# Kernel tuning notes

Hardware: AMD Instinct MI355X
Metric: run time of the kernel (lower is better)

The kernel has to match this reference:

```python
import jax, jax.numpy as jnp
import numpy as np

DN = ('NCHW', 'OIHW', 'NCHW')
EPS = 1e-5


def _conv(x, w, b, stride, pad):
    y = jax.lax.conv_general_dilated(x, w, (stride, stride), ((pad, pad), (pad, pad)), dimension_numbers=DN)
    return y + b[None, :, None, None]


def _convT(x, w, b):
    # PyTorch ConvTranspose2d(k=4, s=2, p=1); w: (Cin, Cout, 4, 4)
    k = jnp.flip(w, (2, 3)).transpose(1, 0, 2, 3)  # -> (Cout, Cin, 4, 4)
    y = jax.lax.conv_general_dilated(x, k, (1, 1), ((2, 2), (2, 2)), lhs_dilation=(2, 2), dimension_numbers=DN)
    return y + b[None, :, None, None]


def _bn(x, g, b):
    # training-mode BatchNorm2d: batch stats over (N, H, W)
    m = x.mean((0, 2, 3), keepdims=True)
    v = x.var((0, 2, 3), keepdims=True)
    return (x - m) * jax.lax.rsqrt(v + EPS) * g[None, :, None, None] + b[None, :, None, None]


def _resblock(x, g1, b1, w3, b3, g2, b2, w1, b1c):
    h = jax.nn.relu(_bn(x, g1, b1))
    h = _conv(h, w3, b3, 1, 1)
    h = jax.nn.relu(_bn(h, g2, b2))
    h = _conv(h, w1, b1c, 1, 0)
    return h + x


def setup_inputs() -> dict:
    B, C, H, W, D, K = 16, 3, 128, 128, 256, 512
    key = jax.random.key(0)
    ks = iter(jax.random.split(key, 16))
    s = 0.05
    inp = {
        'x': jax.random.normal(next(ks), (B, C, H, W), jnp.float32),
        'ec1_w': jax.random.normal(next(ks), (D, C, 4, 4), jnp.float32) * s,
        'ec1_b': jnp.zeros((D,), jnp.float32),
        'ebn1_g': jnp.ones((D,), jnp.float32),
        'ebn1_b': jnp.zeros((D,), jnp.float32),
        'ec2_w': jax.random.normal(next(ks), (D, D, 4, 4), jnp.float32) * s,
        'ec2_b': jnp.zeros((D,), jnp.float32),
        # 4 residual blocks stacked: [0,1]=encoder, [2,3]=decoder
        'rb_bn1_g': jnp.ones((4, D), jnp.float32),
        'rb_bn1_b': jnp.zeros((4, D), jnp.float32),
        'rb_c3_w': jax.random.normal(next(ks), (4, D, D, 3, 3), jnp.float32) * s,
        'rb_c3_b': jnp.zeros((4, D), jnp.float32),
        'rb_bn2_g': jnp.ones((4, D), jnp.float32),
        'rb_bn2_b': jnp.zeros((4, D), jnp.float32),
        'rb_c1_w': jax.random.normal(next(ks), (4, D, D, 1, 1), jnp.float32) * s,
        'rb_c1_b': jnp.zeros((4, D), jnp.float32),
        'dbn1_g': jnp.ones((D,), jnp.float32),
        'dbn1_b': jnp.zeros((D,), jnp.float32),
        'dct1_w': jax.random.normal(next(ks), (D, D, 4, 4), jnp.float32) * s,  # (Cin, Cout, kH, kW)
        'dct1_b': jnp.zeros((D,), jnp.float32),
        'dbn2_g': jnp.ones((D,), jnp.float32),
        'dbn2_b': jnp.zeros((D,), jnp.float32),
        'dct2_w': jax.random.normal(next(ks), (D, C, 4, 4), jnp.float32) * s,
        'dct2_b': jnp.zeros((C,), jnp.float32),
        'codebook': jax.random.uniform(next(ks), (K, D), jnp.float32, -1.0 / K, 1.0 / K),
    }
    return inp


def reference(x, ec1_w, ec1_b, ebn1_g, ebn1_b, ec2_w, ec2_b,
              rb_bn1_g, rb_bn1_b, rb_c3_w, rb_c3_b, rb_bn2_g, rb_bn2_b, rb_c1_w, rb_c1_b,
              dbn1_g, dbn1_b, dct1_w, dct1_b, dbn2_g, dbn2_b, dct2_w, dct2_b, codebook):
    def rb(h, i):
        return _resblock(h, rb_bn1_g[i], rb_bn1_b[i], rb_c3_w[i], rb_c3_b[i],
                         rb_bn2_g[i], rb_bn2_b[i], rb_c1_w[i], rb_c1_b[i])

    # Encoder
    h = _conv(x, ec1_w, ec1_b, 2, 1)
    h = jax.nn.relu(_bn(h, ebn1_g, ebn1_b))
    h = _conv(h, ec2_w, ec2_b, 2, 1)
    h = rb(h, 0)
    z_e = rb(h, 1)  # [N, D, H/4, W/4]

    # Vector quantizer: argmin_k sum_d (z - w_k)^2 via norm expansion
    N, D, Hh, Ww = z_e.shape
    ze_f = z_e.transpose(0, 2, 3, 1).reshape(-1, D)  # [M, D]
    d2 = ((ze_f ** 2).sum(1, keepdims=True)
          - 2.0 * ze_f @ codebook.T
          + (codebook ** 2).sum(1)[None, :])  # [M, K]
    q = jnp.argmin(d2, axis=1)
    z_q = codebook[q].reshape(N, Hh, Ww, D).transpose(0, 3, 1, 2)

    # Decoder (takes z_e, per original forward)
    d = rb(z_e, 2)
    d = rb(d, 3)
    d = jax.nn.relu(_bn(d, dbn1_g, dbn1_b))
    d = _convT(d, dct1_w, dct1_b)
    d = jax.nn.relu(_bn(d, dbn2_g, dbn2_b))
    x_rec = _convT(d, dct2_w, dct2_b)

    return (x_rec, z_e, z_q)
```

## Files before the change

kernel.cpp:

```cpp
#include <hip/hip_runtime.h>
#include <stdint.h>

typedef __bf16 bf16_t;
typedef __bf16 bf16x8 __attribute__((ext_vector_type(8)));
typedef float f32x4 __attribute__((ext_vector_type(4)));

#define DEVINL __device__ __forceinline__

DEVINL float bf2f(bf16_t h){ return (float)h; }
DEVINL bf16_t f2bf(float f){ return (bf16_t)f; }

DEVINL void g2l16(const void* g, void* l){
  __builtin_amdgcn_global_load_lds(
      (const __attribute__((address_space(1))) uint32_t*)g,
      (__attribute__((address_space(3))) uint32_t*)l, 16, 0, 0);
}

#define SB_BYTES    9469952
#define SB0_OFF     35684352
#define STATS_OFF   73564160
#define CBN_OFF     73586688
#define WP_OFF      73588736
#define XI_OFF      83320832
#define WS_NEEDED   91709440
#define WP_RB3(i) (1048576 + (i)*655360)
#define WP_RB1(i) (1048576 + (i)*655360 + 589824)
#define WP_CT     3670016
#define WP_CB     4718592
#define WP_EC1    4849664
#define WP_ELEMS  4866048

__global__ __launch_bounds__(256) void k_zero(uint4* __restrict__ p, int n16){
  int i = blockIdx.x*256 + threadIdx.x;
  if (i < n16) p[i] = make_uint4(0,0,0,0);
}

__global__ __launch_bounds__(256) void k_zerohalo(bf16_t* __restrict__ buf, int IW, int total){
  int idx = blockIdx.x*256 + threadIdx.x;
  if (idx >= total) return;
  int g8 = idx & 31, r = idx >> 5;
  int H = 4*IW - 4;
  int nn = r / H, hp = r - nn*H;
  int y, x;
  if (hp < IW){ y = 0; x = hp; }
  else if (hp < 2*IW){ y = IW-1; x = hp - IW; }
  else {
    int h2 = hp - 2*IW;
    int side = h2 / (IW-2);
    int k = h2 - side*(IW-2);
    y = k + 1; x = side ? (IW-1) : 0;
  }
  bf16_t* p = buf + ((size_t)((nn*IW + y)*IW + x))*256 + g8*8;
  bf16x8 zv;
#pragma unroll
  for (int e = 0; e < 8; e++) zv[e] = f2bf(0.f);
  *(bf16x8*)p = zv;
}

__global__ __launch_bounds__(256) void k_repack(
    const float* __restrict__ ec2_w, const float* __restrict__ rb_c3_w,
    const float* __restrict__ rb_c1_w, const float* __restrict__ dct1_w,
    const float* __restrict__ codebook, const float* __restrict__ ec1_w,
    bf16_t* __restrict__ wp)
{
  int idx = blockIdx.x*256 + threadIdx.x;
  if (idx >= WP_ELEMS) return;
  int l = idx; float v;
  if (l < 1048576) {
    int t = l>>16, co = (l>>8)&255, ci = l&255;
    v = ec2_w[co*4096 + ci*16 + t];
  } else {
    l -= 1048576;
    if (l < 2621440) {
      int i = l / 655360;
      int r = l - i*655360;
      if (r < 589824) {
        int t = r>>16, co = (r>>8)&255, ci = r&255;
        v = rb_c3_w[i*589824 + co*2304 + ci*9 + t];
      } else {
        r -= 589824;
        int co = r>>8, ci = r&255;
        v = rb_c1_w[i*65536 + co*256 + ci];
      }
    } else {
      l -= 2621440;
      if (l < 1048576) {
        int z = l>>18, r = l&262143, t = r>>16, co = (r>>8)&255, ci = r&255;
        int py = z>>1, px = z&1, a = t>>1, b = t&1;
        int ky = 2*a + 1 - py, kx = 2*b + 1 - px;
        v = dct1_w[ci*4096 + co*16 + ky*4 + kx];
      } else {
        l -= 1048576;
        if (l < 131072) {
          v = codebook[l];
        } else {
          l -= 131072;
          int co = l>>6, k = l&63;
          v = (k < 48) ? ec1_w[co*48 + k] : 0.f;
        }
      }
    }
  }
  wp[idx] = f2bf(v);
}

__global__ __launch_bounds__(256) void k_cbnorm(const float* __restrict__ cb, float* __restrict__ out){
  int k = blockIdx.x*256 + threadIdx.x;
  float s = 0.f;
  for (int d = 0; d < 256; d++){ float v = cb[k*256 + d]; s += v*v; }
  out[k] = s;
}

__global__ __launch_bounds__(256) void k_im2col(const float* __restrict__ x, bf16_t* __restrict__ Xi){
  int m = blockIdx.x*256 + threadIdx.x;
  int nn = m >> 12, oy = (m >> 6) & 63, ox = m & 63;
  bf16_t row[64];
#pragma unroll
  for (int k = 48; k < 64; k++) row[k] = f2bf(0.f);
#pragma unroll
  for (int ci = 0; ci < 3; ci++)
#pragma unroll
    for (int ky = 0; ky < 4; ky++){
      int iy = 2*oy + ky - 1;
      bool yok = (unsigned)iy < 128u;
#pragma unroll
      for (int kx = 0; kx < 4; kx++){
        int ix = 2*ox + kx - 1;
        float v = (yok && (unsigned)ix < 128u) ? x[((size_t)((nn*3+ci)*128 + iy))*128 + ix] : 0.f;
        row[ci*16 + ky*4 + kx] = f2bf(v);
      }
    }
#pragma unroll
  for (int u = 0; u < 8; u++){
    bf16x8 o;
#pragma unroll
    for (int e = 0; e < 8; e++) o[e] = row[u*8+e];
    *(bf16x8*)(Xi + (size_t)m*64 + u*8) = o;
  }
}

__global__ __launch_bounds__(256) void k_bnapply(const bf16_t* __restrict__ in, bf16_t* __restrict__ out,
    const float* __restrict__ stat, const float* __restrict__ g, const float* __restrict__ b,
    int hwlog, float invc)
{
  int idx = blockIdx.x*256 + threadIdx.x;
  int g8 = idx & 31, p = idx >> 5;
  int HW = 1 << hwlog, IW = HW + 2;
  int xx = p & (HW-1), yy = (p >> hwlog) & (HW-1), nn = p >> (2*hwlog);
  size_t a = ((size_t)((nn*IW + yy+1)*IW + xx+1))*256 + g8*8;
  float sm[8], sq[8], gv[8], bv[8];
#pragma unroll
  for (int e = 0; e < 8; e += 4){
    *(float4*)(sm+e) = *(const float4*)(stat + g8*8 + e);
    *(float4*)(sq+e) = *(const float4*)(stat + 256 + g8*8 + e);
    *(float4*)(gv+e) = *(const float4*)(g + g8*8 + e);
    *(float4*)(bv+e) = *(const float4*)(b + g8*8 + e);
  }
  bf16x8 v = *(const bf16x8*)(in + a);
  bf16x8 o;
#pragma unroll
  for (int e = 0; e < 8; e++){
    float mean = sm[e]*invc;
    float var  = sq[e]*invc - mean*mean;
    float sc = gv[e] * rsqrtf(var + 1e-5f);
    float sh = bv[e] - mean*sc;
    o[e] = f2bf(fmaxf(bf2f(v[e])*sc + sh, 0.f));
  }
  *(bf16x8*)(out + a) = o;
}

template<int MODE>
__global__ __launch_bounds__(256) void k_gemm(
    const bf16_t* __restrict__ in, const bf16_t* __restrict__ wp,
    const float* __restrict__ bias, const bf16_t* __restrict__ res,
    bf16_t* __restrict__ outb, float* __restrict__ outf,
    float* __restrict__ stat, int out_mode, float alpha)
{
  constexpr int TAPS = (MODE==0)?16:(MODE==1)?9:(MODE==2)?1:(MODE==3)?4:1;
  constexpr int CHUNKS = (MODE==5)?1:TAPS*4;
  const int N = gridDim.y * 64;

  __shared__ __align__(16) bf16_t As[128*64];
  __shared__ __align__(16) bf16_t Bs[64*64];
  __shared__ float s_sum[64], s_sum2[64];

  const int tid  = threadIdx.x;
  const int lane = tid & 63;
  const int wave = tid >> 6;
  const int m0   = blockIdx.x * 128;
  const int n0   = blockIdx.y * 64;
  int py = 0, px = 0;
  const bf16_t* wpp = wp;
  if (MODE == 3){ py = blockIdx.z >> 1; px = blockIdx.z & 1; wpp += (size_t)blockIdx.z * 262144; }

  int abase[4];
#pragma unroll
  for (int j = 0; j < 4; j++){
    int s = j*256 + wave*64 + lane;
    int row = s >> 3, ug = (s & 7) ^ (row & 7);
    int m = m0 + row;
    int pbase;
    if (MODE == 0){ int nn=m>>10, sp=m&1023, oy=sp>>5, ox=sp&31; pbase = (nn*66 + 2*oy)*66 + 2*ox; }
    else if (MODE == 3){ int nn=m>>10, sp=m&1023, oy=sp>>5, ox=sp&31; pbase = (nn*34 + oy+1+py)*34 + ox+1+px; }
    else if (MODE == 5){ pbase = 0; }
    else { int nn=m>>10, sp=m&1023, oy=sp>>5, ox=sp&31; pbase = (nn*34 + oy)*34 + ox; }
    abase[j] = (MODE==5) ? (m*64 + ug*8) : (pbase*256 + ug*8);
  }
  int bbase[2];
#pragma unroll
  for (int j = 0; j < 2; j++){
    int s = j*256 + wave*64 + lane;
    int row = s >> 3, ug = (s & 7) ^ (row & 7);
    bbase[j] = (MODE==5) ? ((n0+row)*64 + ug*8) : ((n0+row)*256 + ug*8);
  }

  f32x4 acc[4][2];
#pragma unroll
  for (int i = 0; i < 4; i++)
#pragma unroll
    for (int j = 0; j < 2; j++) acc[i][j] = (f32x4){0.f,0.f,0.f,0.f};

  const int rowbase = (wave >> 1) * 64;
  const int colbase = (wave & 1) * 32;
  const int mf = lane & 15;
  const int kq = lane >> 4;

  for (int c = 0; c < CHUNKS; ++c){
    int t = (MODE==5) ? 0 : (c >> 2);
    int koff;
    if (MODE == 0)      koff = ((t >> 2)*66 + (t & 3))*256 + ((c&3)<<6);
    else if (MODE == 1){ int ky = t/3; koff = (ky*34 + (t - ky*3))*256 + ((c&3)<<6); }
    else if (MODE == 2) koff = 35*256 + ((c&3)<<6);
    else if (MODE == 3) koff = -((t >> 1)*34 + (t & 1))*256 + ((c&3)<<6);
    else                koff = 0;
    size_t bko = (MODE==5) ? 0 : ((size_t)t*N*256 + ((c&3)<<6));
#pragma unroll
    for (int j = 0; j < 4; j++)
      g2l16(in + abase[j] + koff, As + (j*256 + wave*64)*8);
#pragma unroll
    for (int j = 0; j < 2; j++)
      g2l16(wpp + bko + bbase[j], Bs + (j*256 + wave*64)*8);
    __syncthreads();

#pragma unroll
    for (int kk = 0; kk < 2; kk++){
      bf16x8 af[4], bfr[2];
#pragma unroll
      for (int i = 0; i < 4; i++){
        int rr = rowbase + i*16 + mf;
        af[i] = *reinterpret_cast<const bf16x8*>(&As[rr*64 + (((kk*4+kq) ^ (rr&7))<<3)]);
      }
#pragma unroll
      for (int j = 0; j < 2; j++){
        int rr = colbase + j*16 + mf;
        bfr[j] = *reinterpret_cast<const bf16x8*>(&Bs[rr*64 + (((kk*4+kq) ^ (rr&7))<<3)]);
      }
#pragma unroll
      for (int i = 0; i < 4; i++)
#pragma unroll
        for (int j = 0; j < 2; j++)
          acc[i][j] = __builtin_amdgcn_mfma_f32_16x16x32_bf16(af[i], bfr[j], acc[i][j], 0, 0, 0);
    }
    __syncthreads();
  }

  float psum[2] = {0.f, 0.f}, psum2[2] = {0.f, 0.f};
  const int rowq = (lane >> 4) * 4;
#pragma unroll
  for (int i = 0; i < 4; i++){
#pragma unroll
    for (int r = 0; r < 4; r++){
      int m = m0 + rowbase + i*16 + rowq + r;
      int nn, oy, ox;
      if (MODE == 5){ nn = m >> 12; oy = (m >> 6) & 63; ox = m & 63; }
      else { nn = m >> 10; oy = (m >> 5) & 31; ox = m & 31; }
#pragma unroll
      for (int j = 0; j < 2; j++){
        int co = n0 + colbase + j*16 + mf;
        float v = alpha * acc[i][j][r] + bias[co];
        if (res) v += bf2f(res[((size_t)((nn*34 + oy+1)*34 + ox+1))*256 + co]);
        psum[j] += v; psum2[j] += v*v;
        if (out_mode == 2){
          outf[(size_t)m * N + co] = v;
        } else if (MODE == 3){
          outb[((size_t)((nn*66 + 2*oy+py+1)*66 + 2*ox+px+1))*256 + co] = f2bf(v);
        } else if (MODE == 5){
          outb[((size_t)((nn*66 + oy+1)*66 + ox+1))*256 + co] = f2bf(v);
        } else {
          outb[((size_t)((nn*34 + oy+1)*34 + ox+1))*256 + co] = f2bf(v);
          if (out_mode == 1)
            outf[(size_t)nn*262144 + (size_t)co*1024 + oy*32 + ox] = v;
        }
      }
    }
  }
  if (stat){
    if (tid < 64){ s_sum[tid] = 0.f; s_sum2[tid] = 0.f; }
    __syncthreads();
#pragma unroll
    for (int j = 0; j < 2; j++){
      int cl = colbase + j*16 + mf;
      atomicAdd(&s_sum[cl], psum[j]);
      atomicAdd(&s_sum2[cl], psum2[j]);
    }
    __syncthreads();
    if (tid < 64){
      atomicAdd(&stat[n0 + tid], s_sum[tid]);
      atomicAdd(&stat[256 + n0 + tid], s_sum2[tid]);
    }
  }
}

__global__ __launch_bounds__(256) void k_vq_argmin(const float* __restrict__ scores,
    const float* __restrict__ cb, float* __restrict__ zq)
{
  __shared__ int best[32];
  __shared__ float Z[32*256];
  int tid = threadIdx.x, lane = tid & 63, wave = tid >> 6;
  int m0 = blockIdx.x * 32;
  int nn = m0 >> 10, y = (m0 >> 5) & 31;
  for (int rr = wave; rr < 32; rr += 4){
    const float* srow = scores + (size_t)(m0 + rr) * 512;
    float bv = 3.4e38f; int bk = 0;
    for (int k = lane; k < 512; k += 64){
      float v = srow[k];
      if (v < bv){ bv = v; bk = k; }
    }
    for (int off = 32; off; off >>= 1){
      float ov = __shfl_down(bv, off);
      int   ok = __shfl_down(bk, off);
      if (ov < bv || (ov == bv && ok < bk)){ bv = ov; bk = ok; }
    }
    if (lane == 0) best[rr] = bk;
  }
  __syncthreads();
  for (int rr = 0; rr < 32; rr++)
    Z[rr*256 + tid] = cb[best[rr]*256 + tid];
  __syncthreads();
  float* orow = zq + (size_t)nn*262144 + (size_t)tid*1024 + y*32;
#pragma unroll
  for (int x4 = 0; x4 < 8; x4++){
    float4 v;
    v.x = Z[(x4*4+0)*256 + tid];
    v.y = Z[(x4*4+1)*256 + tid];
    v.z = Z[(x4*4+2)*256 + tid];
    v.w = Z[(x4*4+3)*256 + tid];
    *(float4*)(orow + x4*4) = v;
  }
}

__global__ __launch_bounds__(256) void k_convt2(const bf16_t* __restrict__ A, const float* __restrict__ w,
    const float* __restrict__ bias, const float* __restrict__ stat,
    const float* __restrict__ g, const float* __restrict__ b, float* __restrict__ out)
{
  __shared__ float sc_s[256], sh_s[256];
  int tid = threadIdx.x;
  {
    float mean = stat[tid] * (1.f/65536.f);
    float var  = stat[256+tid] * (1.f/65536.f) - mean*mean;
    float s = g[tid] * rsqrtf(var + 1e-5f);
    sc_s[tid] = s; sh_s[tid] = b[tid] - mean*s;
  }
  __syncthreads();
  int m = blockIdx.x*256 + tid;
  int nn = m >> 12, oyh = (m >> 6) & 63, oxh = m & 63;
  float acc[4][3];
#pragma unroll
  for (int p = 0; p < 4; p++)
#pragma unroll
    for (int co = 0; co < 3; co++) acc[p][co] = bias[co];

  const bf16_t* ipp[9]; bool vv[9];
#pragma unroll
  for (int dy = 0; dy < 3; dy++)
#pragma unroll
    for (int dx = 0; dx < 3; dx++){
      int h = oyh + dy, ww = oxh + dx;
      vv[dy*3+dx] = (h >= 1 && h <= 64 && ww >= 1 && ww <= 64);
      ipp[dy*3+dx] = A + ((size_t)((nn*66 + h)*66 + ww))*256;
    }

  static const int cnt_[3] = {1,2,1};
  static const int pys_[3][2] = {{0,0},{0,1},{1,0}};
  static const int kys_[3][2] = {{3,0},{1,2},{0,0}};

  for (int c8 = 0; c8 < 32; c8++){
    float sc[8], sh[8];
#pragma unroll
    for (int e = 0; e < 8; e += 4){
      *(float4*)(sc+e) = *(const float4*)(sc_s + c8*8 + e);
      *(float4*)(sh+e) = *(const float4*)(sh_s + c8*8 + e);
    }
#pragma unroll
    for (int dy = 0; dy < 3; dy++)
#pragma unroll
      for (int dx = 0; dx < 3; dx++){
        if (!vv[dy*3+dx]) continue;
        bf16x8 hv = *reinterpret_cast<const bf16x8*>(ipp[dy*3+dx] + c8*8);
#pragma unroll
        for (int e = 0; e < 8; e++){
          int ci = c8*8 + e;
          float f = fmaxf(bf2f(hv[e])*sc[e] + sh[e], 0.f);
#pragma unroll
          for (int iy = 0; iy < cnt_[dy]; iy++){
            int py = pys_[dy][iy], ky = kys_[dy][iy];
#pragma unroll
            for (int ix = 0; ix < cnt_[dx]; ix++){
              int px = pys_[dx][ix], kx = kys_[dx][ix];
#pragma unroll
              for (int co = 0; co < 3; co++)
                acc[py*2+px][co] += f * w[ci*48 + co*16 + ky*4 + kx];
            }
          }
        }
      }
  }
#pragma unroll
  for (int py = 0; py < 2; py++)
#pragma unroll
    for (int px = 0; px < 2; px++)
#pragma unroll
      for (int co = 0; co < 3; co++)
        out[(size_t)nn*49152 + (size_t)co*16384 + (size_t)(2*oyh+py)*128 + (2*oxh+px)] = acc[py*2+px][co];
}

extern "C" void kernel_launch(void* const* d_in, const int* in_sizes, int n_in,
                              void* d_out, int out_size, void* d_ws, size_t ws_size,
                              hipStream_t stream)
{
  if (ws_size < (size_t)WS_NEEDED) return;

  const float* x       = (const float*)d_in[0];
  const float* ec1_w   = (const float*)d_in[1];
  const float* ec1_b   = (const float*)d_in[2];
  const float* ebn1_g  = (const float*)d_in[3];
  const float* ebn1_b  = (const float*)d_in[4];
  const float* ec2_w   = (const float*)d_in[5];
  const float* ec2_b   = (const float*)d_in[6];
  const float* rb_bn1_g= (const float*)d_in[7];
  const float* rb_bn1_b= (const float*)d_in[8];
  const float* rb_c3_w = (const float*)d_in[9];
  const float* rb_c3_b = (const float*)d_in[10];
  const float* rb_bn2_g= (const float*)d_in[11];
  const float* rb_bn2_b= (const float*)d_in[12];
  const float* rb_c1_w = (const float*)d_in[13];
  const float* rb_c1_b = (const float*)d_in[14];
  const float* dbn1_g  = (const float*)d_in[15];
  const float* dbn1_b  = (const float*)d_in[16];
  const float* dct1_w  = (const float*)d_in[17];
  const float* dct1_b  = (const float*)d_in[18];
  const float* dbn2_g  = (const float*)d_in[19];
  const float* dbn2_b  = (const float*)d_in[20];
  const float* dct2_w  = (const float*)d_in[21];
  const float* dct2_b  = (const float*)d_in[22];
  const float* codebook= (const float*)d_in[23];

  char* ws = (char*)d_ws;
  bf16_t* A64 = (bf16_t*)ws;
  float*  scores = (float*)ws;
  bf16_t* SB0 = (bf16_t*)(ws + SB0_OFF);
  bf16_t* SB1 = (bf16_t*)(ws + SB0_OFF + 1*SB_BYTES);
  bf16_t* SB2 = (bf16_t*)(ws + SB0_OFF + 2*SB_BYTES);
  bf16_t* SB3 = (bf16_t*)(ws + SB0_OFF + 3*SB_BYTES);
  float*  stats = (float*)(ws + STATS_OFF);
  float*  cbn   = (float*)(ws + CBN_OFF);
  bf16_t* Wp    = (bf16_t*)(ws + WP_OFF);
  bf16_t* Xi    = (bf16_t*)(ws + XI_OFF);

  float* xrec = (float*)d_out;
  float* zef  = xrec + 786432;
  float* zqf  = zef + 4194304;

  k_zerohalo<<<dim3(521), 256, 0, stream>>>(A64, 66, 133120);
  k_zerohalo<<<dim3(264), 256, 0, stream>>>(SB0, 34, 67584);
  k_zerohalo<<<dim3(264), 256, 0, stream>>>(SB1, 34, 67584);
  k_zerohalo<<<dim3(264), 256, 0, stream>>>(SB2, 34, 67584);
  k_zerohalo<<<dim3(264), 256, 0, stream>>>(SB3, 34, 67584);
  k_zero  <<<dim3(6),     256, 0, stream>>>((uint4*)(ws + STATS_OFF), 1408);
  k_repack<<<dim3(19008), 256, 0, stream>>>(ec2_w, rb_c3_w, rb_c1_w, dct1_w, codebook, ec1_w, Wp);
  k_cbnorm<<<dim3(2),     256, 0, stream>>>(codebook, cbn);

  k_im2col<<<dim3(256), 256, 0, stream>>>(x, Xi);
  k_gemm<5><<<dim3(512,4,1), 256, 0, stream>>>(Xi, Wp + WP_EC1, ec1_b, nullptr, A64, nullptr,
                                               stats, 0, 1.f);
  k_bnapply<<<dim3(8192), 256, 0, stream>>>(A64, A64, stats, ebn1_g, ebn1_b, 6, 1.f/65536.f);
  k_gemm<0><<<dim3(128,4,1), 256, 0, stream>>>(A64, Wp, ec2_b, nullptr, SB0, nullptr,
                                               stats + 1*512, 0, 1.f);

  auto launch_rb = [&](bf16_t* xin, bf16_t* xout, int i, int sIn, int sMid, int sOut, float* zf){
    k_bnapply<<<dim3(2048), 256, 0, stream>>>(xin, SB1, stats + sIn*512,
                                              rb_bn1_g + i*256, rb_bn1_b + i*256, 5, 1.f/16384.f);
    k_gemm<1><<<dim3(128,4,1), 256, 0, stream>>>(SB1, Wp + WP_RB3(i), rb_c3_b + i*256,
                                                 nullptr, SB2, nullptr, stats + sMid*512, 0, 1.f);
    k_bnapply<<<dim3(2048), 256, 0, stream>>>(SB2, SB2, stats + sMid*512,
                                              rb_bn2_g + i*256, rb_bn2_b + i*256, 5, 1.f/16384.f);
    k_gemm<2><<<dim3(128,4,1), 256, 0, stream>>>(SB2, Wp + WP_RB1(i), rb_c1_b + i*256,
                                                 xin, xout, zf, stats + sOut*512, zf ? 1 : 0, 1.f);
  };

  launch_rb(SB0, SB3, 0, 1, 2, 3, nullptr);
  launch_rb(SB3, SB0, 1, 3, 4, 5, zef);

  k_gemm<2><<<dim3(128,8,1), 256, 0, stream>>>(SB0, Wp + WP_CB, cbn, nullptr, nullptr, scores,
                                               nullptr, 2, -2.f);
  k_vq_argmin<<<dim3(512), 256, 0, stream>>>(scores, codebook, zqf);
  k_zerohalo<<<dim3(521), 256, 0, stream>>>(A64, 66, 133120);

  launch_rb(SB0, SB3, 2, 5, 6, 7, nullptr);
  launch_rb(SB3, SB0, 3, 7, 8, 9, nullptr);

  k_bnapply<<<dim3(2048), 256, 0, stream>>>(SB0, SB0, stats + 9*512, dbn1_g, dbn1_b, 5, 1.f/16384.f);
  k_gemm<3><<<dim3(128,4,4), 256, 0, stream>>>(SB0, Wp + WP_CT, dct1_b, nullptr, A64, nullptr,
                                               stats + 10*512, 0, 1.f);

  k_convt2<<<dim3(256), 256, 0, stream>>>(A64, dct2_w, dct2_b, stats + 10*512, dbn2_g, dbn2_b, xrec);
}
```

Measured before the change: 796.7 us.

## Move final transposed conv onto MFMA GEMM plus tap-assembly kernel

Replaces the scalar per-pixel final ConvTranspose kernel with three steps: a BN+ReLU apply pass, a bf16 MFMA GEMM that computes all 48 (cout, ky, kx) partial products per input pixel into a float buffer, and a small kernel that sums the four relevant taps per output pixel with bias. Setup kernels (halo zeroing, stats zeroing, codebook norms) are merged into fewer launches, and a redundant re-zeroing of the halo is dropped. This trades the scalar FMA loop for matrix-core work plus an extra float intermediate write and read, and the N dimension is padded to 64.

After: 733.8 us. 7.9% less time.

```diff
diff --git a/kernel.cpp b/kernel.cpp
--- a/kernel.cpp
+++ b/kernel.cpp
@@ -21,23 +21,17 @@
 #define STATS_OFF   73564160
 #define CBN_OFF     73586688
 #define WP_OFF      73588736
-#define XI_OFF      83320832
-#define WS_NEEDED   91709440
+#define XI_OFF      83353600
+#define WS_NEEDED   91742208
 #define WP_RB3(i) (1048576 + (i)*655360)
 #define WP_RB1(i) (1048576 + (i)*655360 + 589824)
 #define WP_CT     3670016
 #define WP_CB     4718592
 #define WP_EC1    4849664
-#define WP_ELEMS  4866048
-
-__global__ __launch_bounds__(256) void k_zero(uint4* __restrict__ p, int n16){
-  int i = blockIdx.x*256 + threadIdx.x;
-  if (i < n16) p[i] = make_uint4(0,0,0,0);
-}
-
-__global__ __launch_bounds__(256) void k_zerohalo(bf16_t* __restrict__ buf, int IW, int total){
-  int idx = blockIdx.x*256 + threadIdx.x;
-  if (idx >= total) return;
+#define WP_CT2    4866048
+#define WP_ELEMS  4882432
+
+DEVINL void zerohalo_one(bf16_t* buf, int IW, int idx){
   int g8 = idx & 31, r = idx >> 5;
   int H = 4*IW - 4;
   int nn = r / H, hp = r - nn*H;
@@ -57,14 +51,39 @@
   *(bf16x8*)p = zv;
 }
 
+__global__ __launch_bounds__(256) void k_prep(bf16_t* __restrict__ A64, bf16_t* __restrict__ SB,
+                                              uint4* __restrict__ statz){
+  int b = blockIdx.x, t = threadIdx.x;
+  if (b < 521){
+    int idx = b*256 + t;
+    if (idx < 133120) zerohalo_one(A64, 66, idx);
+  } else if (b < 1577){
+    int r = b - 521;
+    int buf = r / 264, li = r - buf*264;
+    int idx = li*256 + t;
+    if (idx < 67584) zerohalo_one(SB + (size_t)buf*(SB_BYTES/2), 34, idx);
+  } else {
+    int i = (b - 1577)*256 + t;
+    if (i < 1408) statz[i] = make_uint4(0,0,0,0);
+  }
+}
+
 __global__ __launch_bounds__(256) void k_repack(
     const float* __restrict__ ec2_w, const float* __restrict__ rb_c3_w,
     const float* __restrict__ rb_c1_w, const float* __restrict__ dct1_w,
     const float* __restrict__ codebook, const float* __restrict__ ec1_w,
-    bf16_t* __restrict__ wp)
+    const float* __restrict__ dct2_w, bf16_t* __restrict__ wp, float* __restrict__ cbn)
 {
   int idx = blockIdx.x*256 + threadIdx.x;
-  if (idx >= WP_ELEMS) return;
+  if (idx >= WP_ELEMS){
+    int k = idx - WP_ELEMS;
+    if (k < 512){
+      float s = 0.f;
+      for (int d = 0; d < 256; d++){ float v = codebook[k*256 + d]; s += v*v; }
+      cbn[k] = s;
+    }
+    return;
+  }
   int l = idx; float v;
   if (l < 1048576) {
     int t = l>>16, co = (l>>8)&255, ci = l&255;
@@ -95,20 +114,19 @@
           v = codebook[l];
         } else {
           l -= 131072;
-          int co = l>>6, k = l&63;
-          v = (k < 48) ? ec1_w[co*48 + k] : 0.f;
+          if (l < 16384){
+            int co = l>>6, k = l&63;
+            v = (k < 48) ? ec1_w[co*48 + k] : 0.f;
+          } else {
+            l -= 16384;
+            int n = l>>8, ci = l&255;
+            v = (n < 48) ? dct2_w[ci*48 + n] : 0.f;
+          }
         }
       }
     }
   }
   wp[idx] = f2bf(v);
-}
-
-__global__ __launch_bounds__(256) void k_cbnorm(const float* __restrict__ cb, float* __restrict__ out){
-  int k = blockIdx.x*256 + threadIdx.x;
-  float s = 0.f;
-  for (int d = 0; d < 256; d++){ float v = cb[k*256 + d]; s += v*v; }
-  out[k] = s;
 }
 
 __global__ __launch_bounds__(256) void k_im2col(const float* __restrict__ x, bf16_t* __restrict__ Xi){
@@ -176,7 +194,7 @@
     bf16_t* __restrict__ outb, float* __restrict__ outf,
     float* __restrict__ stat, int out_mode, float alpha)
 {
-  constexpr int TAPS = (MODE==0)?16:(MODE==1)?9:(MODE==2)?1:(MODE==3)?4:1;
+  constexpr int TAPS = (MODE==0)?16:(MODE==1)?9:(MODE==3)?4:1;
   constexpr int CHUNKS = (MODE==5)?1:TAPS*4;
   const int N = gridDim.y * 64;
 
@@ -203,6 +221,7 @@
     if (MODE == 0){ int nn=m>>10, sp=m&1023, oy=sp>>5, ox=sp&31; pbase = (nn*66 + 2*oy)*66 + 2*ox; }
     else if (MODE == 3){ int nn=m>>10, sp=m&1023, oy=sp>>5, ox=sp&31; pbase = (nn*34 + oy+1+py)*34 + ox+1+px; }
     else if (MODE == 5){ pbase = 0; }
+    else if (MODE == 6){ int nn=m>>12, oy=(m>>6)&63, ox=m&63; pbase = (nn*66 + oy+1)*66 + ox+1; }
     else { int nn=m>>10, sp=m&1023, oy=sp>>5, ox=sp&31; pbase = (nn*34 + oy)*34 + ox; }
     abase[j] = (MODE==5) ? (m*64 + ug*8) : (pbase*256 + ug*8);
   }
@@ -232,6 +251,7 @@
     else if (MODE == 1){ int ky = t/3; koff = (ky*34 + (t - ky*3))*256 + ((c&3)<<6); }
     else if (MODE == 2) koff = 35*256 + ((c&3)<<6);
     else if (MODE == 3) koff = -((t >> 1)*34 + (t & 1))*256 + ((c&3)<<6);
+    else if (MODE == 6) koff = ((c&3)<<6);
     else                koff = 0;
     size_t bko = (MODE==5) ? 0 : ((size_t)t*N*256 + ((c&3)<<6));
 #pragma unroll
@@ -277,7 +297,7 @@
 #pragma unroll
       for (int j = 0; j < 2; j++){
         int co = n0 + colbase + j*16 + mf;
-        float v = alpha * acc[i][j][r] + bias[co];
+        float v = alpha * acc[i][j][r] + (bias ? bias[co] : 0.f);
         if (res) v += bf2f(res[((size_t)((nn*34 + oy+1)*34 + ox+1))*256 + co]);
         psum[j] += v; psum2[j] += v*v;
         if (out_mode == 2){
@@ -349,79 +369,31 @@
   }
 }
 
-__global__ __launch_bounds__(256) void k_convt2(const bf16_t* __restrict__ A, const float* __restrict__ w,
-    const float* __restrict__ bias, const float* __restrict__ stat,
-    const float* __restrict__ g, const float* __restrict__ b, float* __restrict__ out)
-{
-  __shared__ float sc_s[256], sh_s[256];
-  int tid = threadIdx.x;
-  {
-    float mean = stat[tid] * (1.f/65536.f);
-    float var  = stat[256+tid] * (1.f/65536.f) - mean*mean;
-    float s = g[tid] * rsqrtf(var + 1e-5f);
-    sc_s[tid] = s; sh_s[tid] = b[tid] - mean*s;
-  }
-  __syncthreads();
-  int m = blockIdx.x*256 + tid;
-  int nn = m >> 12, oyh = (m >> 6) & 63, oxh = m & 63;
-  float acc[4][3];
-#pragma unroll
-  for (int p = 0; p < 4; p++)
-#pragma unroll
-    for (int co = 0; co < 3; co++) acc[p][co] = bias[co];
-
-  const bf16_t* ipp[9]; bool vv[9];
-#pragma unroll
-  for (int dy = 0; dy < 3; dy++)
-#pragma unroll
-    for (int dx = 0; dx < 3; dx++){
-      int h = oyh + dy, ww = oxh + dx;
-      vv[dy*3+dx] = (h >= 1 && h <= 64 && ww >= 1 && ww <= 64);
-      ipp[dy*3+dx] = A + ((size_t)((nn*66 + h)*66 + ww))*256;
-    }
-
-  static const int cnt_[3] = {1,2,1};
-  static const int pys_[3][2] = {{0,0},{0,1},{1,0}};
-  static const int kys_[3][2] = {{3,0},{1,2},{0,0}};
-
-  for (int c8 = 0; c8 < 32; c8++){
-    float sc[8], sh[8];
-#pragma unroll
-    for (int e = 0; e < 8; e += 4){
-      *(float4*)(sc+e) = *(const float4*)(sc_s + c8*8 + e);
-      *(float4*)(sh+e) = *(const float4*)(sh_s + c8*8 + e);
-    }
-#pragma unroll
-    for (int dy = 0; dy < 3; dy++)
-#pragma unroll
-      for (int dx = 0; dx < 3; dx++){
-        if (!vv[dy*3+dx]) continue;
-        bf16x8 hv = *reinterpret_cast<const bf16x8*>(ipp[dy*3+dx] + c8*8);
-#pragma unroll
-        for (int e = 0; e < 8; e++){
-          int ci = c8*8 + e;
-          float f = fmaxf(bf2f(hv[e])*sc[e] + sh[e], 0.f);
-#pragma unroll
-          for (int iy = 0; iy < cnt_[dy]; iy++){
-            int py = pys_[dy][iy], ky = kys_[dy][iy];
-#pragma unroll
-            for (int ix = 0; ix < cnt_[dx]; ix++){
-              int px = pys_[dx][ix], kx = kys_[dx][ix];
-#pragma unroll
-              for (int co = 0; co < 3; co++)
-                acc[py*2+px][co] += f * w[ci*48 + co*16 + ky*4 + kx];
-            }
-          }
-        }
-      }
-  }
-#pragma unroll
-  for (int py = 0; py < 2; py++)
-#pragma unroll
-    for (int px = 0; px < 2; px++)
-#pragma unroll
-      for (int co = 0; co < 3; co++)
-        out[(size_t)nn*49152 + (size_t)co*16384 + (size_t)(2*oyh+py)*128 + (2*oxh+px)] = acc[py*2+px][co];
+__global__ __launch_bounds__(256) void k_ct2asm(const float* __restrict__ P,
+    const float* __restrict__ bias, float* __restrict__ out)
+{
+  int idx = blockIdx.x*256 + threadIdx.x;
+  int nn = idx >> 14, oy2 = (idx >> 7) & 127, ox2 = idx & 127;
+  int py = oy2 & 1, px = ox2 & 1, oyh = oy2 >> 1, oxh = ox2 >> 1;
+  float a0 = bias[0], a1 = bias[1], a2 = bias[2];
+#pragma unroll
+  for (int a = 0; a < 2; a++){
+    int iy = oyh + py - a;
+    if ((unsigned)iy > 63u) continue;
+    int ky = 2*a + 1 - py;
+#pragma unroll
+    for (int b = 0; b < 2; b++){
+      int ix = oxh + px - b;
+      if ((unsigned)ix > 63u) continue;
+      int kx = 2*b + 1 - px;
+      const float* pr = P + ((size_t)(nn*4096 + iy*64 + ix))*64 + ky*4 + kx;
+      a0 += pr[0]; a1 += pr[16]; a2 += pr[32];
+    }
+  }
+  size_t o = (size_t)nn*49152 + (size_t)oy2*128 + ox2;
+  out[o]         = a0;
+  out[o + 16384] = a1;
+  out[o + 32768] = a2;
 }
 
 extern "C" void kernel_launch(void* const* d_in, const int* in_sizes, int n_in,
@@ -462,6 +434,7 @@
   bf16_t* SB1 = (bf16_t*)(ws + SB0_OFF + 1*SB_BYTES);
   bf16_t* SB2 = (bf16_t*)(ws + SB0_OFF + 2*SB_BYTES);
   bf16_t* SB3 = (bf16_t*)(ws + SB0_OFF + 3*SB_BYTES);
+  float*  P   = (float*)(ws + SB0_OFF + 1*SB_BYTES);
   float*  stats = (float*)(ws + STATS_OFF);
   float*  cbn   = (float*)(ws + CBN_OFF);
   bf16_t* Wp    = (bf16_t*)(ws + WP_OFF);
@@ -471,14 +444,9 @@
   float* zef  = xrec + 786432;
   float* zqf  = zef + 4194304;
 
-  k_zerohalo<<<dim3(521), 256, 0, stream>>>(A64, 66, 133120);
-  k_zerohalo<<<dim3(264), 256, 0, stream>>>(SB0, 34, 67584);
-  k_zerohalo<<<dim3(264), 256, 0, stream>>>(SB1, 34, 67584);
-  k_zerohalo<<<dim3(264), 256, 0, stream>>>(SB2, 34, 67584);
-  k_zerohalo<<<dim3(264), 256, 0, stream>>>(SB3, 34, 67584);
-  k_zero  <<<dim3(6),     256, 0, stream>>>((uint4*)(ws + STATS_OFF), 1408);
-  k_repack<<<dim3(19008), 256, 0, stream>>>(ec2_w, rb_c3_w, rb_c1_w, dct1_w, codebook, ec1_w, Wp);
-  k_cbnorm<<<dim3(2),     256, 0, stream>>>(codebook, cbn);
+  k_prep  <<<dim3(1583),  256, 0, stream>>>(A64, SB0, (uint4*)(ws + STATS_OFF));
+  k_repack<<<dim3(19074), 256, 0, stream>>>(ec2_w, rb_c3_w, rb_c1_w, dct1_w, codebook,
+                                            ec1_w, dct2_w, Wp, cbn);
 
   k_im2col<<<dim3(256), 256, 0, stream>>>(x, Xi);
   k_gemm<5><<<dim3(512,4,1), 256, 0, stream>>>(Xi, Wp + WP_EC1, ec1_b, nullptr, A64, nullptr,
@@ -504,7 +472,6 @@
   k_gemm<2><<<dim3(128,8,1), 256, 0, stream>>>(SB0, Wp + WP_CB, cbn, nullptr, nullptr, scores,
                                                nullptr, 2, -2.f);
   k_vq_argmin<<<dim3(512), 256, 0, stream>>>(scores, codebook, zqf);
-  k_zerohalo<<<dim3(521), 256, 0, stream>>>(A64, 66, 133120);
 
   launch_rb(SB0, SB3, 2, 5, 6, 7, nullptr);
   launch_rb(SB3, SB0, 3, 7, 8, 9, nullptr);
@@ -513,5 +480,8 @@
   k_gemm<3><<<dim3(128,4,4), 256, 0, stream>>>(SB0, Wp + WP_CT, dct1_b, nullptr, A64, nullptr,
                                                stats + 10*512, 0, 1.f);
 
-  k_convt2<<<dim3(256), 256, 0, stream>>>(A64, dct2_w, dct2_b, stats + 10*512, dbn2_g, dbn2_b, xrec);
-}
+  k_bnapply<<<dim3(8192), 256, 0, stream>>>(A64, A64, stats + 10*512, dbn2_g, dbn2_b, 6, 1.f/65536.f);
+  k_gemm<6><<<dim3(512,1,1), 256, 0, stream>>>(A64, Wp + WP_CT2, nullptr, nullptr, nullptr, P,
+                                               nullptr, 2, 1.f);
+  k_ct2asm<<<dim3(1024), 256, 0, stream>>>(P, dct2_b, xrec);
+}
```
